# Kernel optimization log

Measured on AMD Instinct MI355X. Metric: run time of the kernel, lower is better.

## Reference

```python
import jax, jax.numpy as jnp
import numpy as np

B, T, C = 2, 4096, 1024
H, M, CHUNK = 16, 64, 128
D = C // H
DELTA = 1e-6


def setup_inputs() -> dict:
    key = jax.random.key(0)
    ks = jax.random.split(key, 4)
    x = jax.random.normal(ks[0], (B, T, C), dtype=jnp.float32)
    Wqkv = jax.random.normal(ks[1], (3 * C, C), dtype=jnp.float32) * 0.02
    bqkv = jnp.zeros((3 * C,), dtype=jnp.float32)
    Wout = jax.random.normal(ks[2], (C, C), dtype=jnp.float32) * 0.02
    bout = jnp.zeros((C,), dtype=jnp.float32)
    proj = jax.random.normal(ks[3], (H, D, M), dtype=jnp.float32) / np.sqrt(D)
    return {"x": x, "Wqkv": Wqkv, "bqkv": bqkv, "Wout": Wout, "bout": bout, "proj": proj}


def reference(x, Wqkv, bqkv, Wout, bout, proj):
    b, t, c = x.shape
    qkv = x @ Wqkv.T + bqkv                      # (B,T,3C)
    q, k, v = jnp.split(qkv, 3, axis=-1)
    # (B,T,C) -> (B,H,T,D)
    def to_heads(z):
        return z.reshape(b, t, H, D).transpose(0, 2, 1, 3).astype(jnp.float32)
    q, k, v = to_heads(q), to_heads(k), to_heads(v)

    nch = t // CHUNK
    # (B,H,T,D) -> (nch, B, H, Tc, D)
    def to_chunks(z):
        return z.reshape(b, H, nch, CHUNK, D).transpose(2, 0, 1, 3, 4)
    qc, kc, vc = to_chunks(q), to_chunks(k), to_chunks(v)

    mask = jnp.tril(jnp.ones((CHUNK, CHUNK), dtype=jnp.float32))

    def step(carry, inp):
        kv_state, k_state = carry                 # (B,H,M,D), (B,H,M)
        q_ch, k_ch, v_ch = inp                    # (B,H,Tc,D)
        qp = jax.nn.relu(jnp.einsum('bhtd,hdm->bhtm', q_ch, proj))
        kp = jax.nn.relu(jnp.einsum('bhtd,hdm->bhtm', k_ch, proj))
        ctx_hist = jnp.einsum('bhtm,bhmd->bhtd', qp, kv_state)
        norm_hist = jnp.einsum('bhtm,bhm->bht', qp, k_state)
        aw = jnp.einsum('bhtm,bhsm->bhts', qp, kp) * mask  # causal intra-chunk
        ctx_intra = jnp.einsum('bhts,bhsd->bhtd', aw, v_ch)
        norm_intra = aw.sum(-1)
        out = (ctx_hist + ctx_intra) / (norm_hist + norm_intra + DELTA)[..., None]
        new_kv = kv_state + jnp.einsum('bhtm,bhtd->bhmd', kp, v_ch)
        new_k = k_state + kp.sum(2)
        return (new_kv, new_k), out

    carry0 = (jnp.zeros((b, H, M, D), jnp.float32), jnp.zeros((b, H, M), jnp.float32))
    _, outs = jax.lax.scan(step, carry0, (qc, kc, vc))  # (nch,B,H,Tc,D)
    out = outs.transpose(1, 2, 0, 3, 4).reshape(b, H, t, D)  # (B,H,T,D)
    out = out.transpose(0, 2, 1, 3).reshape(b, t, c)          # (B,T,C)
    return out @ Wout.T + bout
```

## Files before the change

kernel.cpp:

```cpp
#include <hip/hip_runtime.h>
#include <stdint.h>

#define HN 16
#define DH 64
#define MF 64
#define CHK 128
#define NCH 32
#define TSEQ 4096
#define CIN 1024
#define C3 3072

typedef __attribute__((ext_vector_type(8))) short bf16x8;
typedef __attribute__((ext_vector_type(4))) float f32x4;

__device__ __forceinline__ unsigned short f2b(float f){
  union{float f;uint32_t u;} v; v.f=f;
  return (unsigned short)((v.u + 0x7fffu + ((v.u>>16)&1u))>>16);
}

#define MFMA(a,b,c) __builtin_amdgcn_mfma_f32_16x16x32_bf16(a,b,c,0,0,0)

typedef __attribute__((address_space(1))) void gbl_t;
typedef __attribute__((address_space(3))) void lds_t;
__device__ __forceinline__ void gload_lds16(const void* g, void* l){
  __builtin_amdgcn_global_load_lds((const gbl_t*)g, (lds_t*)l, 16, 0, 0);
}

__global__ __launch_bounds__(256) void cvt_kernel(const float* __restrict__ src,
                                                  unsigned short* __restrict__ dst, int n4){
  int i = blockIdx.x*256 + threadIdx.x;
  if (i >= n4) return;
  float4 v = ((const float4*)src)[i];
  uint64_t pk = (uint64_t)f2b(v.x) | ((uint64_t)f2b(v.y)<<16)
              | ((uint64_t)f2b(v.z)<<32) | ((uint64_t)f2b(v.w)<<48);
  *(uint64_t*)(dst + (size_t)i*4) = pk;
}

__global__ __launch_bounds__(256) void projt_kernel(const float* __restrict__ proj,
                                                    unsigned short* __restrict__ projT){
  int i = blockIdx.x*256 + threadIdx.x;
  if (i >= HN*DH*MF) return;
  int h = i>>12, r = i&4095, d = r>>6, m = r&63;
  projT[(h<<12) + (m<<6) + d] = f2b(proj[i]);
}

template<int OUT_BF16, int KK>
__global__ __launch_bounds__(512, 2) void gemm8p_kernel(
    const unsigned short* __restrict__ A, const unsigned short* __restrict__ Bt,
    const float* __restrict__ bias, void* __restrict__ Cout,
    int Nn, int nbN)
{
  static_assert(KK % 128 == 0, "KK multiple of 128");
  constexpr int NT = KK / 64;
  constexpr int NI = NT / 2;
  static_assert((NT & (NT-1)) == 0, "NT pow2 for wrap");

  __shared__ unsigned short sA[2*256*64];
  __shared__ unsigned short sB[2*256*64];

  int tid = threadIdx.x;
  int w = tid>>6, l = tid&63, g = l>>4, r16 = l&15;
  int wr = w>>2, wc = w&3;

  int nwg = gridDim.x;
  int qq = nwg>>3;
  int wgid = (blockIdx.x & 7)*qq + (blockIdx.x>>3);
  int brow = (wgid / nbN)<<8;
  int bcol = (wgid % nbN)<<8;

  int rofs = tid>>3;
  int cofs = ((tid&7) ^ ((tid>>3)&7))<<3;

  const unsigned short* Ab = A + (size_t)brow*KK;
  const unsigned short* Bb = Bt + (size_t)bcol*KK;
  char* sAc = (char*)sA;
  char* sBc = (char*)sB;

  f32x4 acc[8][4];
  #pragma unroll
  for (int m=0;m<8;m++)
    #pragma unroll
    for (int n=0;n<4;n++) acc[m][n] = (f32x4){0.f,0.f,0.f,0.f};

  auto stgA = [&](int buf, int half, int kt){
    int r0 = half<<7;
    const unsigned short* gp = Ab + (size_t)(r0 + rofs)*KK + (kt<<6) + cofs;
    char* lp = sAc + (buf<<15) + (r0<<7) + (tid<<4);
    gload_lds16(gp, lp);
    gload_lds16(gp + (size_t)64*KK, lp + 64*128);
  };
  auto stgB = [&](int buf, int half, int kt){
    int r0 = half<<7;
    const unsigned short* gp = Bb + (size_t)(r0 + rofs)*KK + (kt<<6) + cofs;
    char* lp = sBc + (buf<<15) + (r0<<7) + (tid<<4);
    gload_lds16(gp, lp);
    gload_lds16(gp + (size_t)64*KK, lp + 64*128);
  };

#define PHASE(BUF, MH, NH, STAGES, GUARD) do{                                      \
    bf16x8 af[4][2], bfv[2][2];                                                    \
    const char* sab = sAc + ((BUF)<<15);                                           \
    const char* sbb = sBc + ((BUF)<<15);                                           \
    _Pragma("unroll")                                                              \
    for (int mf_=0; mf_<4; mf_++){                                                 \
      int row = (MH)*128 + wr*64 + mf_*16 + r16;                                   \
      _Pragma("unroll")                                                            \
      for (int ks_=0; ks_<2; ks_++)                                                \
        af[mf_][ks_] = *(const bf16x8*)(sab + row*128 + (((ks_*4+g)^(r16&7))<<4)); \
    }                                                                              \
    _Pragma("unroll")                                                              \
    for (int nf_=0; nf_<2; nf_++){                                                 \
      int row = (NH)*128 + wc*32 + nf_*16 + r16;                                   \
      _Pragma("unroll")                                                            \
      for (int ks_=0; ks_<2; ks_++)                                                \
        bfv[nf_][ks_] = *(const bf16x8*)(sbb + row*128 + (((ks_*4+g)^(r16&7))<<4));\
    }                                                                              \
    STAGES;                                                                        \
    GUARD;                                                                         \
    __builtin_amdgcn_s_barrier();                                                  \
    __builtin_amdgcn_sched_barrier(0);                                             \
    __builtin_amdgcn_s_setprio(1);                                                 \
    _Pragma("unroll")                                                              \
    for (int mf_=0; mf_<4; mf_++)                                                  \
      _Pragma("unroll")                                                            \
      for (int nf_=0; nf_<2; nf_++)                                                \
        _Pragma("unroll")                                                          \
        for (int ks_=0; ks_<2; ks_++)                                              \
          acc[(MH)*4+mf_][(NH)*2+nf_] =                                            \
            MFMA(af[mf_][ks_], bfv[nf_][ks_], acc[(MH)*4+mf_][(NH)*2+nf_]);        \
    __builtin_amdgcn_s_setprio(0);                                                 \
    __builtin_amdgcn_sched_barrier(0);                                             \
    __builtin_amdgcn_s_barrier();                                                  \
    asm volatile("" ::: "memory");                                                 \
  }while(0)

#define VM4 asm volatile("s_waitcnt vmcnt(4)" ::: "memory")

  stgA(0,0,0); stgA(0,1,0); stgB(0,0,0); stgB(0,1,0);
  stgA(1,0,1); stgB(1,0,1);
  VM4;
  __builtin_amdgcn_s_barrier();
  asm volatile("" ::: "memory");

  for (int it=0; it<NI; ++it){
    int t1 = 2*it+1;
    int t2 = (2*it+2) & (NT-1);
    int t3 = (2*it+3) & (NT-1);
    PHASE(0, 0,0, { stgA(1,1,t1); stgB(1,1,t1); }, {});
    PHASE(0, 0,1, {}, {});
    PHASE(0, 1,0, { stgA(0,0,t2); }, {});
    PHASE(0, 1,1, { stgB(0,0,t2); }, VM4);
    PHASE(1, 0,0, { stgA(0,1,t2); stgB(0,1,t2); }, {});
    PHASE(1, 0,1, {}, {});
    PHASE(1, 1,0, { stgA(1,0,t3); }, {});
    PHASE(1, 1,1, { stgB(1,0,t3); }, VM4);
  }
#undef PHASE
#undef VM4

  #pragma unroll
  for (int n=0;n<4;n++){
    int colg = bcol + (n>>1)*128 + wc*32 + (n&1)*16 + r16;
    float bv = bias[colg];
    #pragma unroll
    for (int m=0;m<8;m++){
      int rowg = brow + (m>>2)*128 + wr*64 + (m&3)*16 + g*4;
      #pragma unroll
      for (int j=0;j<4;j++){
        float v = acc[m][n][j] + bv;
        if (OUT_BF16) ((unsigned short*)Cout)[(size_t)(rowg+j)*Nn + colg] = f2b(v);
        else          ((float*)Cout)[(size_t)(rowg+j)*Nn + colg] = v;
      }
    }
  }
}

__global__ __launch_bounds__(256) void chunk_stats_kernel(
    const unsigned short* __restrict__ qkvb,
    const unsigned short* __restrict__ projT,
    float* __restrict__ Sbuf, float* __restrict__ ssum)
{
  __shared__ unsigned short s_pT[64*64];
  __shared__ unsigned short s_kpT[64*128];
  __shared__ unsigned short s_vT[64*128];
  __shared__ float s_part[256];

  int bid = blockIdx.x;
  int ch = bid&31, h = (bid>>5)&15, b = bid>>9;
  int tid = threadIdx.x, w = tid>>6, l = tid&63, g = l>>4, r16 = l&15;
  int rowbase = b*TSEQ + ch*CHK;
  const unsigned short* kg = qkvb + (size_t)rowbase*C3 + CIN   + h*DH;
  const unsigned short* vg = qkvb + (size_t)rowbase*C3 + 2*CIN + h*DH;

  {
    const unsigned short* p = projT + (h<<12);
    for (int i = tid; i < 4096; i += 256){
      int m = i>>6, d = i&63;
      *(unsigned short*)((char*)s_pT + m*128 + (((d*2) ^ ((m&7)<<4)))) = p[i];
    }
  }
  for (int i = tid; i < 1024; i += 256){
    int t = i>>3, d0 = (i&7)<<3;
    bf16x8 vv = *(const bf16x8*)(vg + (size_t)t*C3 + d0);
    #pragma unroll
    for (int j=0;j<8;j++){
      int d = d0+j;
      *(unsigned short*)((char*)s_vT + d*256 + (((t*2) ^ ((d&15)<<4)))) = (unsigned short)vv[j];
    }
  }
  __syncthreads();

  f32x4 kacc[2][4];
  #pragma unroll
  for (int tr=0;tr<2;tr++)
    #pragma unroll
    for (int nc=0;nc<4;nc++) kacc[tr][nc] = (f32x4){0.f,0.f,0.f,0.f};
  #pragma unroll
  for (int ks=0; ks<2; ks++){
    bf16x8 a[2];
    #pragma unroll
    for (int tr=0;tr<2;tr++){
      int t = w*32 + tr*16 + r16;
      a[tr] = *(const bf16x8*)(kg + (size_t)t*C3 + ks*32 + g*8);
    }
    #pragma unroll
    for (int nc=0;nc<4;nc++){
      int m = nc*16 + r16;
      bf16x8 bb = *(const bf16x8*)((const char*)s_pT + m*128 + (((ks*64 + g*16) ^ ((m&7)<<4))));
      #pragma unroll
      for (int tr=0;tr<2;tr++)
        kacc[tr][nc] = MFMA(a[tr], bb, kacc[tr][nc]);
    }
  }
  #pragma unroll
  for (int nc=0;nc<4;nc++){
    float v = 0.f;
    #pragma unroll
    for (int tr=0;tr<2;tr++)
      #pragma unroll
      for (int j=0;j<4;j++){
        float x = kacc[tr][nc][j]; x = x>0.f?x:0.f;
        v += x;
        int t = w*32 + tr*16 + g*4 + j;
        int m = nc*16 + r16;
        *(unsigned short*)((char*)s_kpT + m*256 + (((t*2) ^ ((m&15)<<4)))) = f2b(x);
      }
    v += __shfl_xor(v,16); v += __shfl_xor(v,32);
    if (g==0) s_part[w*64 + nc*16 + r16] = v;
  }
  __syncthreads();

  f32x4 sacc[4];
  #pragma unroll
  for (int dc=0;dc<4;dc++) sacc[dc] = (f32x4){0.f,0.f,0.f,0.f};
  int mrow = w*16 + r16;
  #pragma unroll
  for (int ks=0; ks<4; ks++){
    bf16x8 a = *(const bf16x8*)((const char*)s_kpT + mrow*256 + (((ks*64 + g*16) ^ ((mrow&15)<<4))));
    #pragma unroll
    for (int dc=0; dc<4; dc++){
      int d = dc*16 + r16;
      bf16x8 bb = *(const bf16x8*)((const char*)s_vT + d*256 + (((ks*64 + g*16) ^ ((d&15)<<4))));
      sacc[dc] = MFMA(a, bb, sacc[dc]);
    }
  }
  float* So = Sbuf + ((size_t)((b*HN + h)*NCH + ch))*4096;
  #pragma unroll
  for (int dc=0; dc<4; dc++)
    #pragma unroll
    for (int j=0;j<4;j++)
      So[(w*16 + g*4 + j)*64 + dc*16 + r16] = sacc[dc][j];
  if (tid < 64){
    float v = s_part[tid] + s_part[64+tid] + s_part[128+tid] + s_part[192+tid];
    ssum[((size_t)((b*HN + h)*NCH + ch))*64 + tid] = v;
  }
}

__global__ __launch_bounds__(256) void scan_kernel(
  const float* __restrict__ Sbuf, const float* __restrict__ ssum,
  float* __restrict__ kvstate, float* __restrict__ kstate)
{
  int bh = blockIdx.x, tid = threadIdx.x;
  const float4* Sp = (const float4*)(Sbuf + (size_t)bh*NCH*4096);
  float4* kvp = (float4*)(kvstate + (size_t)bh*NCH*4096);
  float4 acc[4];
  #pragma unroll
  for (int q=0;q<4;q++) acc[q] = make_float4(0.f,0.f,0.f,0.f);
  for (int c2=0; c2<NCH; c2++){
    #pragma unroll
    for (int q=0;q<4;q++){
      int idx = c2*1024 + q*256 + tid;
      float4 s = Sp[idx];
      kvp[idx] = acc[q];
      acc[q].x += s.x; acc[q].y += s.y; acc[q].z += s.z; acc[q].w += s.w;
    }
  }
  if (tid < 64){
    float a = 0.f;
    const float* sp = ssum + (size_t)bh*NCH*64;
    float* kp2 = kstate + (size_t)bh*NCH*64;
    for (int c2=0;c2<NCH;c2++){ kp2[c2*64+tid] = a; a += sp[c2*64+tid]; }
  }
}

__global__ __launch_bounds__(256) void chunk_out_kernel(
    const unsigned short* __restrict__ qkvb,
    const unsigned short* __restrict__ projT,
    const float* __restrict__ kvstate,
    const float* __restrict__ kstate,
    unsigned short* __restrict__ attnb)
{
  __shared__ unsigned short s_qp[128*64];
  __shared__ unsigned short s_kp[128*64];
  __shared__ unsigned short s_vT[64*128];
  __shared__ unsigned short s_pa[64*64];

  int bid = blockIdx.x;
  int ch = bid&31, h=(bid>>5)&15, b=bid>>9;
  int tid=threadIdx.x, w=tid>>6, l=tid&63, g=l>>4, r16=l&15;
  int rowbase = b*TSEQ + ch*CHK;
  const unsigned short* qg = qkvb + (size_t)rowbase*C3 + h*DH;
  const unsigned short* kg = qg + CIN;
  const unsigned short* vg = qg + 2*CIN;
  const float* kvg = kvstate + ((size_t)((b*HN+h)*NCH + ch))*4096;
  const float* ksg = kstate  + ((size_t)((b*HN+h)*NCH + ch))*64;

  {
    const unsigned short* p = projT + (h<<12);
    for (int i = tid; i < 4096; i += 256){
      int m = i>>6, d = i&63;
      *(unsigned short*)((char*)s_pa + m*128 + (((d*2) ^ ((m&7)<<4)))) = p[i];
    }
  }
  for (int i = tid; i < 1024; i += 256){
    int t = i>>3, d0 = (i&7)<<3;
    bf16x8 vv = *(const bf16x8*)(vg + (size_t)t*C3 + d0);
    #pragma unroll
    for (int j=0;j<8;j++){
      int d = d0+j;
      *(unsigned short*)((char*)s_vT + d*256 + (((t*2) ^ ((d&15)<<4)))) = (unsigned short)vv[j];
    }
  }
  __syncthreads();

  f32x4 qacc[2][4];
  #pragma unroll
  for (int tr=0;tr<2;tr++)
    #pragma unroll
    for (int nc=0;nc<4;nc++) qacc[tr][nc] = (f32x4){0.f,0.f,0.f,0.f};
  #pragma unroll
  for (int ks=0; ks<2; ks++){
    bf16x8 a[2];
    #pragma unroll
    for (int tr=0;tr<2;tr++){
      int t = w*32 + tr*16 + r16;
      a[tr] = *(const bf16x8*)(qg + (size_t)t*C3 + ks*32 + g*8);
    }
    #pragma unroll
    for (int nc=0;nc<4;nc++){
      int m = nc*16 + r16;
      bf16x8 bb = *(const bf16x8*)((const char*)s_pa + m*128 + (((ks*64 + g*16) ^ ((m&7)<<4))));
      #pragma unroll
      for (int tr=0;tr<2;tr++)
        qacc[tr][nc] = MFMA(a[tr], bb, qacc[tr][nc]);
    }
  }
  float nh[2][4];
  #pragma unroll
  for (int tr=0;tr<2;tr++)
    #pragma unroll
    for (int j=0;j<4;j++) nh[tr][j] = 0.f;
  #pragma unroll
  for (int nc=0;nc<4;nc++){
    float ksv = ksg[nc*16 + r16];
    #pragma unroll
    for (int tr=0;tr<2;tr++)
      #pragma unroll
      for (int j=0;j<4;j++){
        float x = qacc[tr][nc][j]; x = x>0.f?x:0.f;
        nh[tr][j] += x*ksv;
        int t = w*32 + tr*16 + g*4 + j;
        int m = nc*16 + r16;
        *(unsigned short*)((char*)s_qp + t*128 + (((m*2) ^ ((t&7)<<4)))) = f2b(x);
      }
  }
  f32x4 kacc[2][4];
  #pragma unroll
  for (int tr=0;tr<2;tr++)
    #pragma unroll
    for (int nc=0;nc<4;nc++) kacc[tr][nc] = (f32x4){0.f,0.f,0.f,0.f};
  #pragma unroll
  for (int ks=0; ks<2; ks++){
    bf16x8 a[2];
    #pragma unroll
    for (int tr=0;tr<2;tr++){
      int t = w*32 + tr*16 + r16;
      a[tr] = *(const bf16x8*)(kg + (size_t)t*C3 + ks*32 + g*8);
    }
    #pragma unroll
    for (int nc=0;nc<4;nc++){
      int m = nc*16 + r16;
      bf16x8 bb = *(const bf16x8*)((const char*)s_pa + m*128 + (((ks*64 + g*16) ^ ((m&7)<<4))));
      #pragma unroll
      for (int tr=0;tr<2;tr++)
        kacc[tr][nc] = MFMA(a[tr], bb, kacc[tr][nc]);
    }
  }
  #pragma unroll
  for (int nc=0;nc<4;nc++)
    #pragma unroll
    for (int tr=0;tr<2;tr++)
      #pragma unroll
      for (int j=0;j<4;j++){
        float x = kacc[tr][nc][j]; x = x>0.f?x:0.f;
        int t = w*32 + tr*16 + g*4 + j;
        int m = nc*16 + r16;
        *(unsigned short*)((char*)s_kp + t*128 + (((m*2) ^ ((t&7)<<4)))) = f2b(x);
      }
  __syncthreads();

  f32x4 ctx[2][4];
  float ni[2][4];
  #pragma unroll
  for (int tr=0;tr<2;tr++){
    #pragma unroll
    for (int dc=0;dc<4;dc++) ctx[tr][dc] = (f32x4){0.f,0.f,0.f,0.f};
    #pragma unroll
    for (int j=0;j<4;j++) ni[tr][j] = 0.f;
  }

  for (int sb=0; sb<4; sb++){
    f32x4 aw[2][2];
    #pragma unroll
    for (int tr=0;tr<2;tr++)
      #pragma unroll
      for (int sc=0;sc<2;sc++) aw[tr][sc] = (f32x4){0.f,0.f,0.f,0.f};
    #pragma unroll
    for (int ks=0; ks<2; ks++){
      bf16x8 a[2];
      #pragma unroll
      for (int tr=0;tr<2;tr++){
        int t = w*32 + tr*16 + r16;
        a[tr] = *(const bf16x8*)((const char*)s_qp + t*128 + (((ks*64 + g*16) ^ ((t&7)<<4))));
      }
      #pragma unroll
      for (int sc=0;sc<2;sc++){
        int s = sb*32 + sc*16 + r16;
        bf16x8 bb = *(const bf16x8*)((const char*)s_kp + s*128 + (((ks*64 + g*16) ^ ((s&7)<<4))));
        #pragma unroll
        for (int tr=0;tr<2;tr++)
          aw[tr][sc] = MFMA(a[tr], bb, aw[tr][sc]);
      }
    }
    #pragma unroll
    for (int tr=0;tr<2;tr++)
      #pragma unroll
      for (int sc=0;sc<2;sc++)
        #pragma unroll
        for (int j=0;j<4;j++){
          int t = w*32 + tr*16 + g*4 + j;
          int s = sb*32 + sc*16 + r16;
          float x = (s<=t)? aw[tr][sc][j] : 0.f;
          ni[tr][j] += x;
          int sl = sc*16 + r16;
          *(unsigned short*)((char*)s_pa + t*64 + (((sl*2) ^ ((t&3)<<4)))) = f2b(x);
        }
    __syncthreads();
    #pragma unroll
    for (int tr=0;tr<2;tr++){
      int t = w*32 + tr*16 + r16;
      bf16x8 a2 = *(const bf16x8*)((const char*)s_pa + t*64 + (((g*16) ^ ((t&3)<<4))));
      #pragma unroll
      for (int dc=0;dc<4;dc++){
        int d = dc*16 + r16;
        bf16x8 bb = *(const bf16x8*)((const char*)s_vT + d*256 + (((sb*64 + g*16) ^ ((d&15)<<4))));
        ctx[tr][dc] = MFMA(a2, bb, ctx[tr][dc]);
      }
    }
    __syncthreads();
  }

  #pragma unroll
  for (int ks=0; ks<2; ks++){
    bf16x8 a[2];
    #pragma unroll
    for (int tr=0;tr<2;tr++){
      int t = w*32 + tr*16 + r16;
      a[tr] = *(const bf16x8*)((const char*)s_qp + t*128 + (((ks*64 + g*16) ^ ((t&7)<<4))));
    }
    #pragma unroll
    for (int dc=0;dc<4;dc++){
      bf16x8 bb;
      #pragma unroll
      for (int i=0;i<8;i++)
        bb[i] = (short)f2b(kvg[(ks*32 + g*8 + i)*64 + dc*16 + r16]);
      #pragma unroll
      for (int tr=0;tr<2;tr++)
        ctx[tr][dc] = MFMA(a[tr], bb, ctx[tr][dc]);
    }
  }

  float nrm[2][4];
  #pragma unroll
  for (int tr=0;tr<2;tr++)
    #pragma unroll
    for (int j=0;j<4;j++){
      float v = nh[tr][j] + ni[tr][j];
      v += __shfl_xor(v,1); v += __shfl_xor(v,2);
      v += __shfl_xor(v,4); v += __shfl_xor(v,8);
      nrm[tr][j] = v + 1e-6f;
    }

  #pragma unroll
  for (int tr=0;tr<2;tr++)
    #pragma unroll
    for (int dc=0;dc<4;dc++)
      #pragma unroll
      for (int j=0;j<4;j++){
        int t = w*32 + tr*16 + g*4 + j;
        int d = dc*16 + r16;
        attnb[(size_t)(rowbase + t)*CIN + h*DH + d] = f2b(ctx[tr][dc][j] / nrm[tr][j]);
      }
}

extern "C" void kernel_launch(void* const* d_in, const int* in_sizes, int n_in,
                              void* d_out, int out_size, void* d_ws, size_t ws_size,
                              hipStream_t stream)
{
  const float* x    = (const float*)d_in[0];
  const float* Wqkv = (const float*)d_in[1];
  const float* bqkv = (const float*)d_in[2];
  const float* Wout = (const float*)d_in[3];
  const float* bout = (const float*)d_in[4];
  const float* proj = (const float*)d_in[5];

  char* ws = (char*)d_ws;
  unsigned short* xb     = (unsigned short*)(ws + 0);
  unsigned short* attnb  = (unsigned short*)(ws + 0);
  unsigned short* wqkvb  = (unsigned short*)(ws + 16777216);
  float*          ssum   = (float*)(ws + 16777216);
  float*          kstate = (float*)(ws + 17039360);
  unsigned short* qkvb   = (unsigned short*)(ws + 23068672);
  unsigned short* woutb  = (unsigned short*)(ws + 73400320);
  unsigned short* projTb = (unsigned short*)(ws + 75497472);
  float*          Sbuf   = (float*)(ws + 75628544);
  float*          kvstate= (float*)(ws + 92405760);

  cvt_kernel<<<8192, 256, 0, stream>>>(x, xb, 2097152);
  cvt_kernel<<<3072, 256, 0, stream>>>(Wqkv, wqkvb, 786432);
  cvt_kernel<<<1024, 256, 0, stream>>>(Wout, woutb, 262144);
  projt_kernel<<<256, 256, 0, stream>>>(proj, projTb);

  gemm8p_kernel<1,1024><<<384, 512, 0, stream>>>(xb, wqkvb, bqkv, qkvb, 3072, 12);

  chunk_stats_kernel<<<1024, 256, 0, stream>>>(qkvb, projTb, Sbuf, ssum);
  scan_kernel<<<32, 256, 0, stream>>>(Sbuf, ssum, kvstate, kstate);
  chunk_out_kernel<<<1024, 256, 0, stream>>>(qkvb, projTb, kvstate, kstate, attnb);

  gemm8p_kernel<0,1024><<<128, 512, 0, stream>>>(attnb, woutb, bout, d_out, 1024, 4);
}
```

Baseline: 191.8 us.

## Shrink GEMM tile to 256x128 and split scan across more blocks

The GEMM kernel's output tile goes from 256x256 to 256x128. The warp layout changes to 2x4 with each warp covering 128 rows by 32 columns, and the LDS-fragment load and MFMA pipeline is restructured around a single B stage per k-tile. This doubles the workgroup count for both projections (768 and 256), so more CUs are busy, notably for the output GEMM that previously launched only 128 blocks. Separately, the state scan splits each (b,h) pair across four blocks, raising its grid from 32 to 128. The trade-off is lower arithmetic intensity per tile and more A-matrix re-reads from global memory.

Measured after the change: 164.5 us. 1.17x faster.

```diff
diff --git a/kernel.cpp b/kernel.cpp
--- a/kernel.cpp
+++ b/kernel.cpp
@@ -56,7 +56,7 @@
   static_assert((NT & (NT-1)) == 0, "NT pow2 for wrap");
 
   __shared__ unsigned short sA[2*256*64];
-  __shared__ unsigned short sB[2*256*64];
+  __shared__ unsigned short sB[2*128*64];
 
   int tid = threadIdx.x;
   int w = tid>>6, l = tid&63, g = l>>4, r16 = l&15;
@@ -66,7 +66,7 @@
   int qq = nwg>>3;
   int wgid = (blockIdx.x & 7)*qq + (blockIdx.x>>3);
   int brow = (wgid / nbN)<<8;
-  int bcol = (wgid % nbN)<<8;
+  int bcol = (wgid % nbN)<<7;
 
   int rofs = tid>>3;
   int cofs = ((tid&7) ^ ((tid>>3)&7))<<3;
@@ -76,95 +76,95 @@
   char* sAc = (char*)sA;
   char* sBc = (char*)sB;
 
-  f32x4 acc[8][4];
+  f32x4 acc[8][2];
   #pragma unroll
   for (int m=0;m<8;m++)
     #pragma unroll
-    for (int n=0;n<4;n++) acc[m][n] = (f32x4){0.f,0.f,0.f,0.f};
+    for (int n=0;n<2;n++) acc[m][n] = (f32x4){0.f,0.f,0.f,0.f};
 
   auto stgA = [&](int buf, int half, int kt){
     int r0 = half<<7;
     const unsigned short* gp = Ab + (size_t)(r0 + rofs)*KK + (kt<<6) + cofs;
     char* lp = sAc + (buf<<15) + (r0<<7) + (tid<<4);
     gload_lds16(gp, lp);
-    gload_lds16(gp + (size_t)64*KK, lp + 64*128);
+    gload_lds16(gp + (size_t)64*KK, lp + 8192);
   };
-  auto stgB = [&](int buf, int half, int kt){
-    int r0 = half<<7;
-    const unsigned short* gp = Bb + (size_t)(r0 + rofs)*KK + (kt<<6) + cofs;
-    char* lp = sBc + (buf<<15) + (r0<<7) + (tid<<4);
+  auto stgB = [&](int buf, int kt){
+    const unsigned short* gp = Bb + (size_t)rofs*KK + (kt<<6) + cofs;
+    char* lp = sBc + (buf<<14) + (tid<<4);
     gload_lds16(gp, lp);
-    gload_lds16(gp + (size_t)64*KK, lp + 64*128);
+    gload_lds16(gp + (size_t)64*KK, lp + 8192);
   };
 
-#define PHASE(BUF, MH, NH, STAGES, GUARD) do{                                      \
-    bf16x8 af[4][2], bfv[2][2];                                                    \
-    const char* sab = sAc + ((BUF)<<15);                                           \
-    const char* sbb = sBc + ((BUF)<<15);                                           \
-    _Pragma("unroll")                                                              \
-    for (int mf_=0; mf_<4; mf_++){                                                 \
-      int row = (MH)*128 + wr*64 + mf_*16 + r16;                                   \
-      _Pragma("unroll")                                                            \
-      for (int ks_=0; ks_<2; ks_++)                                                \
-        af[mf_][ks_] = *(const bf16x8*)(sab + row*128 + (((ks_*4+g)^(r16&7))<<4)); \
-    }                                                                              \
-    _Pragma("unroll")                                                              \
-    for (int nf_=0; nf_<2; nf_++){                                                 \
-      int row = (NH)*128 + wc*32 + nf_*16 + r16;                                   \
-      _Pragma("unroll")                                                            \
-      for (int ks_=0; ks_<2; ks_++)                                                \
-        bfv[nf_][ks_] = *(const bf16x8*)(sbb + row*128 + (((ks_*4+g)^(r16&7))<<4));\
-    }                                                                              \
-    STAGES;                                                                        \
-    GUARD;                                                                         \
-    __builtin_amdgcn_s_barrier();                                                  \
-    __builtin_amdgcn_sched_barrier(0);                                             \
-    __builtin_amdgcn_s_setprio(1);                                                 \
-    _Pragma("unroll")                                                              \
-    for (int mf_=0; mf_<4; mf_++)                                                  \
-      _Pragma("unroll")                                                            \
-      for (int nf_=0; nf_<2; nf_++)                                                \
-        _Pragma("unroll")                                                          \
-        for (int ks_=0; ks_<2; ks_++)                                              \
-          acc[(MH)*4+mf_][(NH)*2+nf_] =                                            \
-            MFMA(af[mf_][ks_], bfv[nf_][ks_], acc[(MH)*4+mf_][(NH)*2+nf_]);        \
-    __builtin_amdgcn_s_setprio(0);                                                 \
-    __builtin_amdgcn_sched_barrier(0);                                             \
-    __builtin_amdgcn_s_barrier();                                                  \
-    asm volatile("" ::: "memory");                                                 \
+  bf16x8 af[4][2];
+  bf16x8 bfv[2][2];
+
+#define LDA(SAB, MH) do{                                                            \
+    _Pragma("unroll")                                                               \
+    for (int mf_=0; mf_<4; mf_++){                                                  \
+      int row_ = wr*128 + (MH)*64 + mf_*16 + r16;                                   \
+      _Pragma("unroll")                                                             \
+      for (int ks_=0; ks_<2; ks_++)                                                 \
+        af[mf_][ks_] = *(const bf16x8*)((SAB) + row_*128 + (((ks_*4+g)^(r16&7))<<4));\
+    } }while(0)
+#define LDB(SBB, NH) do{                                                            \
+    int row_ = wc*32 + (NH)*16 + r16;                                               \
+    _Pragma("unroll")                                                               \
+    for (int ks_=0; ks_<2; ks_++)                                                   \
+      bfv[NH][ks_] = *(const bf16x8*)((SBB) + row_*128 + (((ks_*4+g)^(r16&7))<<4)); \
+    }while(0)
+#define MM(MH, NH) do{                                                              \
+    __builtin_amdgcn_s_barrier();                                                   \
+    __builtin_amdgcn_sched_barrier(0);                                              \
+    __builtin_amdgcn_s_setprio(1);                                                  \
+    _Pragma("unroll")                                                               \
+    for (int mf_=0; mf_<4; mf_++)                                                   \
+      _Pragma("unroll")                                                             \
+      for (int ks_=0; ks_<2; ks_++)                                                 \
+        acc[(MH)*4+mf_][(NH)] = MFMA(af[mf_][ks_], bfv[NH][ks_], acc[(MH)*4+mf_][(NH)]); \
+    __builtin_amdgcn_s_setprio(0);                                                  \
+    __builtin_amdgcn_sched_barrier(0);                                              \
+    __builtin_amdgcn_s_barrier();                                                   \
+    asm volatile("" ::: "memory");                                                  \
   }while(0)
-
-#define VM4 asm volatile("s_waitcnt vmcnt(4)" ::: "memory")
-
-  stgA(0,0,0); stgA(0,1,0); stgB(0,0,0); stgB(0,1,0);
-  stgA(1,0,1); stgB(1,0,1);
-  VM4;
+#define VM2 asm volatile("s_waitcnt vmcnt(2)" ::: "memory")
+
+  const char* a0 = sAc;
+  const char* a1 = sAc + (1<<15);
+  const char* b0 = sBc;
+  const char* b1 = sBc + (1<<14);
+
+  stgA(0,0,0); stgA(0,1,0); stgB(0,0);
+  stgA(1,0,1);
+  VM2;
   __builtin_amdgcn_s_barrier();
   asm volatile("" ::: "memory");
 
   for (int it=0; it<NI; ++it){
-    int t1 = 2*it+1;
-    int t2 = (2*it+2) & (NT-1);
-    int t3 = (2*it+3) & (NT-1);
-    PHASE(0, 0,0, { stgA(1,1,t1); stgB(1,1,t1); }, {});
-    PHASE(0, 0,1, {}, {});
-    PHASE(0, 1,0, { stgA(0,0,t2); }, {});
-    PHASE(0, 1,1, { stgB(0,0,t2); }, VM4);
-    PHASE(1, 0,0, { stgA(0,1,t2); stgB(0,1,t2); }, {});
-    PHASE(1, 0,1, {}, {});
-    PHASE(1, 1,0, { stgA(1,0,t3); }, {});
-    PHASE(1, 1,1, { stgB(1,0,t3); }, VM4);
-  }
-#undef PHASE
-#undef VM4
-
-  #pragma unroll
-  for (int n=0;n<4;n++){
-    int colg = bcol + (n>>1)*128 + wc*32 + (n&1)*16 + r16;
+    int to  = 2*it+1;
+    int tn  = (2*it+2) & (NT-1);
+    int tnn = (2*it+3) & (NT-1);
+    LDA(a0,0); LDB(b0,0); stgA(1,1,to);        MM(0,0);
+    LDB(b0,1);            stgB(1,to);          MM(0,1);
+    LDA(a0,1);            stgA(0,0,tn);        MM(1,1);
+                                         VM2;  MM(1,0);
+    LDA(a1,0); LDB(b1,0); stgA(0,1,tn);        MM(0,0);
+    LDB(b1,1);            stgB(0,tn);          MM(0,1);
+    LDA(a1,1);            stgA(1,0,tnn);       MM(1,1);
+                                         VM2;  MM(1,0);
+  }
+#undef LDA
+#undef LDB
+#undef MM
+#undef VM2
+
+  #pragma unroll
+  for (int n=0;n<2;n++){
+    int colg = bcol + wc*32 + n*16 + r16;
     float bv = bias[colg];
     #pragma unroll
     for (int m=0;m<8;m++){
-      int rowg = brow + (m>>2)*128 + wr*64 + (m&3)*16 + g*4;
+      int rowg = brow + wr*128 + (m>>2)*64 + (m&3)*16 + g*4;
       #pragma unroll
       for (int j=0;j<4;j++){
         float v = acc[m][n][j] + bv;
@@ -280,22 +280,18 @@
   const float* __restrict__ Sbuf, const float* __restrict__ ssum,
   float* __restrict__ kvstate, float* __restrict__ kstate)
 {
-  int bh = blockIdx.x, tid = threadIdx.x;
+  int bh = blockIdx.x>>2, qd = blockIdx.x&3, tid = threadIdx.x;
   const float4* Sp = (const float4*)(Sbuf + (size_t)bh*NCH*4096);
   float4* kvp = (float4*)(kvstate + (size_t)bh*NCH*4096);
-  float4 acc[4];
-  #pragma unroll
-  for (int q=0;q<4;q++) acc[q] = make_float4(0.f,0.f,0.f,0.f);
+  int idx0 = (tid>>2)*16 + qd*4 + (tid&3);
+  float4 acc = make_float4(0.f,0.f,0.f,0.f);
   for (int c2=0; c2<NCH; c2++){
-    #pragma unroll
-    for (int q=0;q<4;q++){
-      int idx = c2*1024 + q*256 + tid;
-      float4 s = Sp[idx];
-      kvp[idx] = acc[q];
-      acc[q].x += s.x; acc[q].y += s.y; acc[q].z += s.z; acc[q].w += s.w;
-    }
-  }
-  if (tid < 64){
+    int idx = c2*1024 + idx0;
+    float4 s = Sp[idx];
+    kvp[idx] = acc;
+    acc.x += s.x; acc.y += s.y; acc.z += s.z; acc.w += s.w;
+  }
+  if (qd==0 && tid < 64){
     float a = 0.f;
     const float* sp = ssum + (size_t)bh*NCH*64;
     float* kp2 = kstate + (size_t)bh*NCH*64;
@@ -551,11 +547,11 @@
   cvt_kernel<<<1024, 256, 0, stream>>>(Wout, woutb, 262144);
   projt_kernel<<<256, 256, 0, stream>>>(proj, projTb);
 
-  gemm8p_kernel<1,1024><<<384, 512, 0, stream>>>(xb, wqkvb, bqkv, qkvb, 3072, 12);
+  gemm8p_kernel<1,1024><<<768, 512, 0, stream>>>(xb, wqkvb, bqkv, qkvb, 3072, 24);
 
   chunk_stats_kernel<<<1024, 256, 0, stream>>>(qkvb, projTb, Sbuf, ssum);
-  scan_kernel<<<32, 256, 0, stream>>>(Sbuf, ssum, kvstate, kstate);
+  scan_kernel<<<128, 256, 0, stream>>>(Sbuf, ssum, kvstate, kstate);
   chunk_out_kernel<<<1024, 256, 0, stream>>>(qkvb, projTb, kvstate, kstate, attnb);
 
-  gemm8p_kernel<0,1024><<<128, 512, 0, stream>>>(attnb, woutb, bout, d_out, 1024, 4);
-}
+  gemm8p_kernel<0,1024><<<256, 512, 0, stream>>>(attnb, woutb, bout, d_out, 1024, 8);
+}
```
